# Kernel tuning notes

Measured on AMD Instinct MI355X. Metric: run time of the kernel, lower is better.

## Reference

```python
import jax, jax.numpy as jnp
import numpy as np

B, V, T = 256, 4, 512
N = 128          # num_notes_per_voice[0]
H = 256          # lstm_hidden_size
HL = 200         # hidden_size_linear
L = 2            # num_layers


def _scalar_lstm_last(x, Wih, Whh, b):
    """Stacked LSTM(input=1, hidden=1, layers=L) over x:(M,T) -> last output (M,).
    Wih, Whh, b: (L, 4) scalar weights per gate (i,f,g,o order, PyTorch biases summed)."""
    M = x.shape[0]
    h0 = jnp.zeros((L, M), x.dtype)
    c0 = jnp.zeros((L, M), x.dtype)

    def step(carry, xt):
        h, c = carry
        inp = xt
        hs, cs = [], []
        for l in range(L):
            g = Wih[l][:, None] * inp[None, :] + Whh[l][:, None] * h[l][None, :] + b[l][:, None]  # (4, M)
            i, f, gg, o = jax.nn.sigmoid(g[0]), jax.nn.sigmoid(g[1]), jnp.tanh(g[2]), jax.nn.sigmoid(g[3])
            cn = f * c[l] + i * gg
            hn = o * jnp.tanh(cn)
            hs.append(hn); cs.append(cn)
            inp = hn
        return (jnp.stack(hs), jnp.stack(cs)), None

    (h, _), _ = jax.lax.scan(step, (h0, c0), x.T)  # scan over time
    return h[-1]  # top layer final hidden, (M,)


def _lstm2_last(x, Wih0, Whh0, b0, Wih1, Whh1, b1):
    """2-layer LSTM(input=1, hidden=H) over x:(B,S,1) -> last top-layer hidden (B,H)."""
    Bs = x.shape[0]
    Hd = Whh0.shape[1]

    def cell(pre, c):
        i, f, g, o = jnp.split(pre, 4, axis=-1)
        cn = jax.nn.sigmoid(f) * c + jax.nn.sigmoid(i) * jnp.tanh(g)
        return jax.nn.sigmoid(o) * jnp.tanh(cn), cn

    z = jnp.zeros((Bs, Hd), x.dtype)

    def step(carry, xt):
        h0, c0, h1, c1 = carry
        h0n, c0n = cell(xt @ Wih0.T + h0 @ Whh0.T + b0, c0)
        h1n, c1n = cell(h0n @ Wih1.T + h1 @ Whh1.T + b1, c1)
        return (h0n, c0n, h1n, c1n), None

    (_, _, h1, _), _ = jax.lax.scan(step, (z, z, z, z), x.transpose(1, 0, 2))
    return h1


def _branch(tokens, tW, tU, tb, Wih0, Whh0, b0, Wih1, Whh1, b1):
    """Fused version of the per-class Python loop: one-hot each of N classes over
    time (voice 0 only, as in the source), run scalar LSTM per (batch, class),
    then 2-layer LSTM over the class axis. tokens: (B, T) int."""
    Bs, Ts = tokens.shape
    onehot = (tokens[:, :, None] == jnp.arange(N)[None, None, :]).astype(jnp.float32)  # (B,T,N)
    x = onehot.transpose(0, 2, 1).reshape(Bs * N, Ts)           # (B*N, T): one series per class
    states = _scalar_lstm_last(x, tW, tU, tb).reshape(Bs, N, 1)  # States_ln / States_rn
    return _lstm2_last(states, Wih0, Whh0, b0, Wih1, Whh1, b1)   # (B, H)


def setup_inputs() -> dict:
    key = jax.random.key(0)
    ks = iter(jax.random.split(key, 32))
    def rn_(shape, s=0.1):
        return jax.random.normal(next(ks), shape, dtype=jnp.float32) * s
    inp = {
        "ln": jax.random.randint(next(ks), (B, V, T), 0, N),
        "cn": jax.random.randint(next(ks), (B, V - 1), 0, N),
        "rn": jax.random.randint(next(ks), (B, V, T), 0, N),
        "metas": jax.random.randint(next(ks), (B, 3, T), 0, 16),
        # time_lstm_left/right: LSTM(1->1), L layers; biases summed into one
        "tl_Wih": rn_((L, 4), 0.5), "tl_Whh": rn_((L, 4), 0.5), "tl_b": rn_((L, 4), 0.5),
        "tr_Wih": rn_((L, 4), 0.5), "tr_Whh": rn_((L, 4), 0.5), "tr_b": rn_((L, 4), 0.5),
        # notes_lstm_left/right: 2-layer LSTM(1->H)
        "nl_Wih0": rn_((4 * H, 1)), "nl_Whh0": rn_((4 * H, H)), "nl_b0": rn_((4 * H,)),
        "nl_Wih1": rn_((4 * H, H)), "nl_Whh1": rn_((4 * H, H)), "nl_b1": rn_((4 * H,)),
        "nr_Wih0": rn_((4 * H, 1)), "nr_Whh0": rn_((4 * H, H)), "nr_b0": rn_((4 * H,)),
        "nr_Wih1": rn_((4 * H, H)), "nr_Whh1": rn_((4 * H, H)), "nr_b1": rn_((4 * H,)),
        # mlp_predictions: Linear(2H -> HL) -> ReLU -> Linear(HL -> N)
        "mW1": rn_((HL, 2 * H)), "mb1": rn_((HL,)),
        "mW2": rn_((N, HL)), "mb2": rn_((N,)),
    }
    return inp


def reference(ln, cn, rn, metas,
              tl_Wih, tl_Whh, tl_b, tr_Wih, tr_Whh, tr_b,
              nl_Wih0, nl_Whh0, nl_b0, nl_Wih1, nl_Whh1, nl_b1,
              nr_Wih0, nr_Whh0, nr_b0, nr_Wih1, nr_Whh1, nr_b1,
              mW1, mb1, mW2, mb2):
    # cn and metas are unpacked but unused in the original forward()
    note_pred_ln = _branch(ln[:, 0, :], tl_Wih, tl_Whh, tl_b,
                           nl_Wih0, nl_Whh0, nl_b0, nl_Wih1, nl_Whh1, nl_b1)
    note_pred_rn = _branch(rn[:, 0, :], tr_Wih, tr_Whh, tr_b,
                           nr_Wih0, nr_Whh0, nr_b0, nr_Wih1, nr_Whh1, nr_b1)
    h = jnp.concatenate([note_pred_ln, note_pred_rn], axis=1)   # (B, 2H)
    return jax.nn.relu(h @ mW1.T + mb1) @ mW2.T + mb2           # (B, N)
```

## Files before the change

### kernel.cpp

```cpp
#include <hip/hip_runtime.h>


typedef _Float16 f16;
typedef __attribute__((ext_vector_type(4))) _Float16 f16x4;
typedef __attribute__((ext_vector_type(8))) _Float16 f16x8;
typedef __attribute__((ext_vector_type(4))) float f32x4;
typedef unsigned long long u64;

#define NBATCH 256
#define NTIME  512
#define NCLS   128
#define NHID   256

__device__ __forceinline__ float sigf(float x) {
    return __builtin_amdgcn_rcpf(1.0f + __expf(-x));
}
__device__ __forceinline__ float tanh_f(float x) {
    return fmaf(2.0f, __builtin_amdgcn_rcpf(1.0f + __expf(-2.0f * x)), -1.0f);
}
__device__ __forceinline__ f16x4 LO(f16x8 v) { f16x4 r; r[0]=v[0]; r[1]=v[1]; r[2]=v[2]; r[3]=v[3]; return r; }
__device__ __forceinline__ f16x4 HI(f16x8 v) { f16x4 r; r[0]=v[4]; r[1]=v[5]; r[2]=v[6]; r[3]=v[7]; return r; }

__device__ __forceinline__ u64 ld_llc(const u64* p) {
    return __hip_atomic_load(p, __ATOMIC_RELAXED, __HIP_MEMORY_SCOPE_AGENT);
}
__device__ __forceinline__ void st_llc(u64* p, u64 v) {
    __hip_atomic_store(p, v, __ATOMIC_RELAXED, __HIP_MEMORY_SCOPE_AGENT);
}
__device__ __forceinline__ int ld_flag(const int* p) {
    return __hip_atomic_load(p, __ATOMIC_RELAXED, __HIP_MEMORY_SCOPE_AGENT);
}
__device__ __forceinline__ void st_flag(int* p, int v) {
    __hip_atomic_store(p, v, __ATOMIC_RELAXED, __HIP_MEMORY_SCOPE_AGENT);
}

struct P6 {
    const float* s0; const float* s1; const float* s2;
    const float* s3; const float* s4; const float* s5;
};

__global__ __launch_bounds__(256) void k_pre(
    const int* __restrict__ ln, const int* __restrict__ rn,
    const float* __restrict__ tlW, const float* __restrict__ tlU, const float* __restrict__ tlb,
    const float* __restrict__ trW, const float* __restrict__ trU, const float* __restrict__ trb,
    float* __restrict__ states,
    P6 p, f16* __restrict__ wdst,
    int* __restrict__ flags)
{
    const int bid = blockIdx.x;
    const int tid = threadIdx.x;
    if (bid >= 768) {
        int* f = flags + (bid - 768) * 16384;
        for (int i = tid; i < 16384; i += 256) f[i] = 0;
        return;
    }
    if (bid >= 256) {
        const int base = (bid - 256) * 3072;
#pragma unroll
        for (int k = 0; k < 12; ++k) {
            const int i = base + k * 256 + tid;
            const int seg = i >> 18, d = i & 262143;
            const float* s = seg == 0 ? p.s0 : seg == 1 ? p.s1 : seg == 2 ? p.s2
                           : seg == 3 ? p.s3 : seg == 4 ? p.s4 : p.s5;
            const int e  = d & 7;
            const int fr = (d >> 3) & 15;
            const int fq = (d >> 7) & 3;
            const int ktp = (d >> 9) & 7;
            const int fi = (d >> 12) & 15;
            const int g  = (d >> 16) & 3;
            const int row = g * 256 + fi * 16 + fr;
            const int col = ktp * 32 + (e >> 2) * 16 + fq * 4 + (e & 3);
            wdst[i] = (f16)s[row * 256 + col];
        }
        return;
    }
    __shared__ int tok[2][NTIME];
    const int half = tid >> 7, n = tid & 127;
    const int pair = bid * 2 + half;
    const int branch = pair >> 8;
    const int b = pair & 255;
    const int* tp = (branch ? rn : ln) + (size_t)b * (4 * NTIME);
    for (int i = n; i < NTIME; i += 128) tok[half][i] = tp[i];
    __syncthreads();
    const float* W  = branch ? trW : tlW;
    const float* U  = branch ? trU : tlU;
    const float* Bb = branch ? trb : tlb;
    const float u00 = U[0], u01 = U[1], u02 = U[2], u03 = U[3];
    const float f00 = Bb[0], f01 = Bb[1], f02 = Bb[2], f03 = Bb[3];
    const float o00 = f00 + W[0], o01 = f01 + W[1], o02 = f02 + W[2], o03 = f03 + W[3];
    const float w10 = W[4], w11 = W[5], w12 = W[6], w13 = W[7];
    const float u10 = U[4], u11 = U[5], u12 = U[6], u13 = U[7];
    const float b10 = Bb[4], b11 = Bb[5], b12 = Bb[6], b13 = Bb[7];
    float h0 = 0.f, c0 = 0.f, h1 = 0.f, c1 = 0.f;
    {
        const bool x = (tok[half][0] == n);
        float pi = fmaf(u00, h0, x ? o00 : f00);
        float pf = fmaf(u01, h0, x ? o01 : f01);
        float pg = fmaf(u02, h0, x ? o02 : f02);
        float po = fmaf(u03, h0, x ? o03 : f03);
        const float ig = sigf(pi), fg = sigf(pf), gg = tanh_f(pg), og = sigf(po);
        c0 = fmaf(fg, c0, ig * gg);
        h0 = og * tanh_f(c0);
    }
    for (int t = 1; t < NTIME; ++t) {
        const bool x = (tok[half][t] == n);
        float api = fmaf(u00, h0, x ? o00 : f00);
        float apf = fmaf(u01, h0, x ? o01 : f01);
        float apg = fmaf(u02, h0, x ? o02 : f02);
        float apo = fmaf(u03, h0, x ? o03 : f03);
        float bpi = fmaf(w10, h0, fmaf(u10, h1, b10));
        float bpf = fmaf(w11, h0, fmaf(u11, h1, b11));
        float bpg = fmaf(w12, h0, fmaf(u12, h1, b12));
        float bpo = fmaf(w13, h0, fmaf(u13, h1, b13));
        const float aig = sigf(api), afg = sigf(apf), agg = tanh_f(apg), aog = sigf(apo);
        const float big = sigf(bpi), bfg = sigf(bpf), bgg = tanh_f(bpg), bog = sigf(bpo);
        c0 = fmaf(afg, c0, aig * agg);
        c1 = fmaf(bfg, c1, big * bgg);
        h0 = aog * tanh_f(c0);
        h1 = bog * tanh_f(c1);
    }
    {
        float pi = fmaf(w10, h0, fmaf(u10, h1, b10));
        float pf = fmaf(w11, h0, fmaf(u11, h1, b11));
        float pg = fmaf(w12, h0, fmaf(u12, h1, b12));
        float po = fmaf(w13, h0, fmaf(u13, h1, b13));
        const float ig = sigf(pi), fg = sigf(pf), gg = tanh_f(pg), og = sigf(po);
        c1 = fmaf(fg, c1, ig * gg);
        h1 = og * tanh_f(c1);
    }
    states[((size_t)(branch * NBATCH + b)) * NCLS + n] = h1;
}

__global__ __launch_bounds__(256, 2) void k_rec(
    const float* __restrict__ states,
    const f16* __restrict__ whh0, const f16* __restrict__ whh1,
    const f16* __restrict__ wih1,
    const float* __restrict__ wih0L, const float* __restrict__ wih0R,
    const float* __restrict__ b0L, const float* __restrict__ b0R,
    const float* __restrict__ b1L, const float* __restrict__ b1R,
    f16* __restrict__ h0img,
    f16* __restrict__ ring,
    int* __restrict__ flags0,
    int* __restrict__ flags1,
    float* __restrict__ h1out)
{
    extern __shared__ char smem[];
    f16*   wlds = (f16*)smem;
    f16*   img  = (f16*)(smem + 65536);
    float* cmb  = (float*)(smem + 73728);

    const int bid = blockIdx.x;
    const bool isL1 = bid >= 256;
    const int sub = isL1 ? (bid - 256) : bid;
    const int qm = sub >> 5, g = sub & 31;
    const int branch = g >> 4, tb = g & 15;
    const int tid = threadIdx.x;
    const int w = tid >> 6, l = tid & 63, fr = l & 15, fq = l >> 4;

    {
        const f16* base = (isL1 ? whh1 : whh0) + ((size_t)branch << 18);
        for (int c = tid; c < 4096; c += 256) {
            const int rl = c >> 6, coli = c & 63;
            const int gg = rl >> 4, ff = (rl >> 3) & 1, ktp = rl & 7;
            *(uint4*)(wlds + rl * 512 + coli * 8) =
                *(const uint4*)(base + ((size_t)((gg * 16 + qm * 2 + ff) * 8 + ktp) << 9) + coli * 8);
        }
    }
    ((uint4*)img)[tid] = (uint4){0u, 0u, 0u, 0u};
    ((uint4*)img)[tid + 256] = (uint4){0u, 0u, 0u, 0u};

    if (!isL1) {
        const float* bias = branch ? b0R : b0L;
        const float* w0p  = branch ? wih0R : wih0L;
        const int fi_f = qm * 2 + (w < 2 ? w : 0);
        float bv[4], w0v[4];
#pragma unroll
        for (int g4 = 0; g4 < 4; ++g4) {
            bv[g4]  = bias[g4 * 256 + fi_f * 16 + fr];
            w0v[g4] = w0p[g4 * 256 + fi_f * 16 + fr];
        }
        float cst[4] = {0.f, 0.f, 0.f, 0.f};
        f16* gimg = h0img + (size_t)g * (NCLS * 4096);
        int* f0 = flags0 + g * 512;
        __syncthreads();

        for (int s = 0; s < NCLS; ++s) {
            float st[4];
            if (w < 2) {
#pragma unroll
                for (int r = 0; r < 4; ++r)
                    st[r] = states[((size_t)(branch * NBATCH + tb * 16 + fq * 4 + r)) * NCLS + s];
            }
            f16x4 af[16];
#pragma unroll
            for (int kt = 0; kt < 16; ++kt)
                af[kt] = *(const f16x4*)(img + kt * 256 + l * 4);
            f32x4 acc[2];
#pragma unroll
            for (int f = 0; f < 2; ++f) {
                f32x4 a0 = {0.f,0.f,0.f,0.f}, a1 = {0.f,0.f,0.f,0.f};
#pragma unroll
                for (int ktp = 0; ktp < 8; ++ktp) {
                    const f16x8 v = *(const f16x8*)(wlds + (((w * 2 + f) * 8 + ktp) << 9) + l * 8);
                    a0 = __builtin_amdgcn_mfma_f32_16x16x16f16(af[2 * ktp],     LO(v), a0, 0, 0, 0);
                    a1 = __builtin_amdgcn_mfma_f32_16x16x16f16(af[2 * ktp + 1], HI(v), a1, 0, 0, 0);
                }
                acc[f] = a0 + a1;
            }
            if (w == 0) {
#pragma unroll
                for (int r = 0; r < 4; ++r) cmb[(0 * 4 + r) * 64 + l] = acc[1][r];
            } else if (w == 1) {
#pragma unroll
                for (int r = 0; r < 4; ++r) cmb[(1 * 4 + r) * 64 + l] = acc[0][r];
            } else if (w == 2) {
#pragma unroll
                for (int r = 0; r < 4; ++r) {
                    cmb[(2 * 4 + r) * 64 + l] = acc[0][r];
                    cmb[(3 * 4 + r) * 64 + l] = acc[1][r];
                }
            } else {
#pragma unroll
                for (int r = 0; r < 4; ++r) {
                    cmb[(4 * 4 + r) * 64 + l] = acc[0][r];
                    cmb[(5 * 4 + r) * 64 + l] = acc[1][r];
                }
            }
            __syncthreads();
            if (w < 2) {
#pragma unroll
                for (int r = 0; r < 4; ++r) {
                    const float g0 = (w == 0) ? acc[0][r] : cmb[(0 * 4 + r) * 64 + l];
                    const float g1 = (w == 0) ? cmb[(1 * 4 + r) * 64 + l] : acc[1][r];
                    const float g2 = (w == 0) ? cmb[(2 * 4 + r) * 64 + l] : cmb[(3 * 4 + r) * 64 + l];
                    const float g3 = (w == 0) ? cmb[(4 * 4 + r) * 64 + l] : cmb[(5 * 4 + r) * 64 + l];
                    const float pi = fmaf(st[r], w0v[0], g0 + bv[0]);
                    const float pf = fmaf(st[r], w0v[1], g1 + bv[1]);
                    const float pg = fmaf(st[r], w0v[2], g2 + bv[2]);
                    const float po = fmaf(st[r], w0v[3], g3 + bv[3]);
                    const float ig = sigf(pi), fg = sigf(pf), gg = tanh_f(pg), og = sigf(po);
                    cst[r] = fmaf(fg, cst[r], ig * gg);
                    const float hn = og * tanh_f(cst[r]);
                    img[fi_f * 256 + (fq * 4 + r + 16 * (fr >> 2)) * 4 + (fr & 3)] = (f16)hn;
                }
            }
            __syncthreads();
            if (w == 0) {
                u64* gd = (u64*)(gimg + (size_t)s * 4096);
                st_llc(gd + qm * 128 + l,      ((const u64*)img)[qm * 128 + l]);
                st_llc(gd + qm * 128 + 64 + l, ((const u64*)img)[qm * 128 + 64 + l]);
                asm volatile("s_waitcnt vmcnt(0)" ::: "memory");
                if (l == 0) st_flag(f0 + qm * 64, s + 1);
                if (s < NCLS - 1 && l < 7) {
                    const int p = l + (l >= qm);
                    while (ld_flag(f0 + p * 64) <= s) __builtin_amdgcn_s_sleep(1);
                }
            }
            if (s == NCLS - 1) break;
            __syncthreads();
            if (tid < 128) {
                const u64* gs = (const u64*)(gimg + (size_t)s * 4096);
                u64 tmp[7];
#pragma unroll
                for (int j = 0; j < 7; ++j) {
                    const int p = j + (j >= qm);
                    tmp[j] = ld_llc(gs + p * 128 + tid);
                }
#pragma unroll
                for (int j = 0; j < 7; ++j) {
                    const int p = j + (j >= qm);
                    ((u64*)img)[p * 128 + tid] = tmp[j];
                }
            }
            __syncthreads();
        }
    } else {
        const float* bias = branch ? b1R : b1L;
        float bv[2][4];
#pragma unroll
        for (int f = 0; f < 2; ++f)
#pragma unroll
            for (int g4 = 0; g4 < 4; ++g4)
                bv[f][g4] = bias[g4 * 256 + (qm * 2 + f) * 16 + fr];
        float cst[2][4] = {{0.f,0.f,0.f,0.f},{0.f,0.f,0.f,0.f}};
        const f16* wstream = wih1 + ((size_t)branch << 18) + l * 8;
        const f16* gimg = h0img + (size_t)g * (NCLS * 4096);
        f16* gring = ring + (size_t)g * (4 * 4096);
        int* f0 = flags0 + g * 512;
        int* f1 = flags1 + g * 512;
        __syncthreads();
        if (w == 1 && l < 8) {
            while (ld_flag(f0 + l * 64) < 1) __builtin_amdgcn_s_sleep(2);
        }
        __syncthreads();
        f16x4 af0[16];
        {
            const u64* s2 = (const u64*)gimg + l;
#pragma unroll
            for (int kt = 0; kt < 16; ++kt)
                af0[kt] = __builtin_bit_cast(f16x4, ld_llc(s2 + kt * 64));
        }

        for (int t = 0; t < NCLS; ++t) {
            f16x8 wv[2][8];
#pragma unroll
            for (int f = 0; f < 2; ++f)
#pragma unroll
                for (int ktp = 0; ktp < 8; ++ktp)
                    wv[f][ktp] = *(const f16x8*)(wstream
                        + ((size_t)((w * 16 + qm * 2 + f) * 8 + ktp) << 9));
            f16x4 af1[16];
#pragma unroll
            for (int kt = 0; kt < 16; ++kt)
                af1[kt] = *(const f16x4*)(img + kt * 256 + l * 4);
            f32x4 acc[2];
#pragma unroll
            for (int f = 0; f < 2; ++f) {
                f32x4 a0 = {0.f,0.f,0.f,0.f}, a1 = {0.f,0.f,0.f,0.f};
#pragma unroll
                for (int ktp = 0; ktp < 8; ++ktp) {
                    const f16x8 v = *(const f16x8*)(wlds + (((w * 2 + f) * 8 + ktp) << 9) + l * 8);
                    a0 = __builtin_amdgcn_mfma_f32_16x16x16f16(af1[2 * ktp],     LO(v), a0, 0, 0, 0);
                    a1 = __builtin_amdgcn_mfma_f32_16x16x16f16(af1[2 * ktp + 1], HI(v), a1, 0, 0, 0);
                }
#pragma unroll
                for (int ktp = 0; ktp < 8; ++ktp) {
                    a0 = __builtin_amdgcn_mfma_f32_16x16x16f16(af0[2 * ktp],     LO(wv[f][ktp]), a0, 0, 0, 0);
                    a1 = __builtin_amdgcn_mfma_f32_16x16x16f16(af0[2 * ktp + 1], HI(wv[f][ktp]), a1, 0, 0, 0);
                }
                acc[f] = a0 + a1;
            }
            if (w > 0) {
#pragma unroll
                for (int f = 0; f < 2; ++f)
#pragma unroll
                    for (int r = 0; r < 4; ++r)
                        cmb[(((w - 1) * 2 + f) * 4 + r) * 64 + l] = acc[f][r];
            }
            __syncthreads();
            if (w == 0) {
#pragma unroll
                for (int f = 0; f < 2; ++f) {
#pragma unroll
                    for (int r = 0; r < 4; ++r) {
                        const float g0 = acc[f][r];
                        const float g1 = cmb[((0 * 2 + f) * 4 + r) * 64 + l];
                        const float g2 = cmb[((1 * 2 + f) * 4 + r) * 64 + l];
                        const float g3 = cmb[((2 * 2 + f) * 4 + r) * 64 + l];
                        const float pi = g0 + bv[f][0];
                        const float pf = g1 + bv[f][1];
                        const float pg = g2 + bv[f][2];
                        const float po = g3 + bv[f][3];
                        const float ig = sigf(pi), fg = sigf(pf), gg = tanh_f(pg), og = sigf(po);
                        cst[f][r] = fmaf(fg, cst[f][r], ig * gg);
                        const float hn = og * tanh_f(cst[f][r]);
                        if (t == NCLS - 1)
                            h1out[((size_t)(branch * NBATCH + tb * 16 + fq * 4 + r)) * NHID
                                  + (qm * 2 + f) * 16 + fr] = hn;
                        else
                            img[(qm * 2 + f) * 256 + (fq * 4 + r + 16 * (fr >> 2)) * 4 + (fr & 3)] = (f16)hn;
                    }
                }
            }
            if (t == NCLS - 1) break;
            f16* slot = gring + (size_t)(t & 3) * 4096;
            if (w == 0) {
                asm volatile("s_waitcnt lgkmcnt(0)" ::: "memory");
                u64* gd = (u64*)slot;
                st_llc(gd + qm * 128 + l,      ((const u64*)img)[qm * 128 + l]);
                st_llc(gd + qm * 128 + 64 + l, ((const u64*)img)[qm * 128 + 64 + l]);
                asm volatile("s_waitcnt vmcnt(0)" ::: "memory");
                if (l == 0) st_flag(f1 + qm * 64, t + 1);
                if (l < 7) {
                    const int p = l + (l >= qm);
                    while (ld_flag(f1 + p * 64) <= t) __builtin_amdgcn_s_sleep(1);
                }
            }
            if (w == 1 && l < 8) {
                while (ld_flag(f0 + l * 64) < t + 2) __builtin_amdgcn_s_sleep(1);
            }
            __syncthreads();
            {
                const u64* s2 = (const u64*)(gimg + (size_t)(t + 1) * 4096) + l;
#pragma unroll
                for (int kt = 0; kt < 16; ++kt)
                    af0[kt] = __builtin_bit_cast(f16x4, ld_llc(s2 + kt * 64));
            }
            if (tid < 128) {
                const u64* gs = (const u64*)slot;
                u64 tmp[7];
#pragma unroll
                for (int j = 0; j < 7; ++j) {
                    const int p = j + (j >= qm);
                    tmp[j] = ld_llc(gs + p * 128 + tid);
                }
#pragma unroll
                for (int j = 0; j < 7; ++j) {
                    const int p = j + (j >= qm);
                    ((u64*)img)[p * 128 + tid] = tmp[j];
                }
            }
            __syncthreads();
        }
    }
}

__global__ __launch_bounds__(256) void k_mlp(
    const float* __restrict__ h1all,
    const float* __restrict__ W1, const float* __restrict__ b1,
    const float* __restrict__ W2, const float* __restrict__ b2,
    float* __restrict__ out)
{
    __shared__ float hrow[512];
    __shared__ float hid[200];
    const int b = blockIdx.x, tid = threadIdx.x;
    hrow[tid]       = h1all[(size_t)b * NHID + tid];
    hrow[256 + tid] = h1all[(size_t)(NBATCH + b) * NHID + tid];
    __syncthreads();
    if (tid < 200) {
        float a = b1[tid];
        const float* wr = W1 + (size_t)tid * 512;
        for (int k = 0; k < 512; ++k) a = fmaf(wr[k], hrow[k], a);
        hid[tid] = fmaxf(a, 0.f);
    }
    __syncthreads();
    if (tid < 128) {
        float a = b2[tid];
        const float* wr = W2 + (size_t)tid * 200;
        for (int j = 0; j < 200; ++j) a = fmaf(wr[j], hid[j], a);
        out[(size_t)b * 128 + tid] = a;
    }
}

extern "C" void kernel_launch(void* const* d_in, const int* in_sizes, int n_in,
                              void* d_out, int out_size, void* d_ws, size_t ws_size,
                              hipStream_t stream)
{
    (void)in_sizes; (void)n_in; (void)out_size; (void)ws_size;
    const int*   ln    = (const int*)d_in[0];
    const int*   rn    = (const int*)d_in[2];
    const float* tlW   = (const float*)d_in[4];
    const float* tlU   = (const float*)d_in[5];
    const float* tlb   = (const float*)d_in[6];
    const float* trW   = (const float*)d_in[7];
    const float* trU   = (const float*)d_in[8];
    const float* trb   = (const float*)d_in[9];
    const float* wih0L = (const float*)d_in[10];
    const float* b0L   = (const float*)d_in[12];
    const float* b1L   = (const float*)d_in[15];
    const float* wih0R = (const float*)d_in[16];
    const float* b0R   = (const float*)d_in[18];
    const float* b1R   = (const float*)d_in[21];
    const float* mW1   = (const float*)d_in[22];
    const float* mb1   = (const float*)d_in[23];
    const float* mW2   = (const float*)d_in[24];
    const float* mb2   = (const float*)d_in[25];

    char* ws = (char*)d_ws;
    f16*   w16    = (f16*)ws;
    float* states = (float*)(ws + 3145728);
    float* h1out  = (float*)(ws + 3407872);
    int*   flags  = (int*)(ws + 3932160);
    f16*   ring   = (f16*)(ws + 4063232);
    f16*   h0img  = (f16*)(ws + 5111808);

    f16* whh0 = w16;
    f16* whh1 = w16 + 2 * 262144;
    f16* wih1 = w16 + 4 * 262144;
    int* flags0 = flags;
    int* flags1 = flags + 16384;

    (void)hipFuncSetAttribute(reinterpret_cast<const void*>(k_rec),
                              hipFuncAttributeMaxDynamicSharedMemorySize, 79872);

    P6 p { (const float*)d_in[11], (const float*)d_in[17],
           (const float*)d_in[14], (const float*)d_in[20],
           (const float*)d_in[13], (const float*)d_in[19] };
    k_pre<<<770, 256, 0, stream>>>(ln, rn, tlW, tlU, tlb, trW, trU, trb,
                                   states, p, w16, flags);
    k_rec<<<512, 256, 79872, stream>>>(states, whh0, whh1, wih1, wih0L, wih0R,
                                       b0L, b0R, b1L, b1R, h0img, ring,
                                       flags0, flags1, h1out);
    k_mlp<<<256, 256, 0, stream>>>(h1out, mW1, mb1, mW2, mb2, (float*)d_out);
}
```

Measured before the change: 640.1 us.

## Split layer-1 gate nonlinearity across two waves and move flag polling off the publisher

In the layer-1 LSTM loop, waves 0 and 1 now each compute the cell update for one of the two feature tiles, where wave 0 previously did both. The gate partial sums are exchanged through a rearranged shared-memory layout to support this. Flag polling for peer blocks moves from wave 0 to waves 2 and 3, so the publishing wave no longer also spins, and the layer-0 loop gets the same polling move. This shortens the serial per-step critical path at the cost of an extra __syncthreads per step.

```diff
diff --git a/kernel.cpp b/kernel.cpp
--- a/kernel.cpp
+++ b/kernel.cpp
@@ -251,10 +251,9 @@
                 st_llc(gd + qm * 128 + 64 + l, ((const u64*)img)[qm * 128 + 64 + l]);
                 asm volatile("s_waitcnt vmcnt(0)" ::: "memory");
                 if (l == 0) st_flag(f0 + qm * 64, s + 1);
-                if (s < NCLS - 1 && l < 7) {
-                    const int p = l + (l >= qm);
-                    while (ld_flag(f0 + p * 64) <= s) __builtin_amdgcn_s_sleep(1);
-                }
+            } else if (w == 2 && s < NCLS - 1 && l < 7) {
+                const int p = l + (l >= qm);
+                while (ld_flag(f0 + p * 64) <= s) __builtin_amdgcn_s_sleep(1);
             }
             if (s == NCLS - 1) break;
             __syncthreads();
@@ -276,20 +275,18 @@
         }
     } else {
         const float* bias = branch ? b1R : b1L;
-        float bv[2][4];
-#pragma unroll
-        for (int f = 0; f < 2; ++f)
-#pragma unroll
-            for (int g4 = 0; g4 < 4; ++g4)
-                bv[f][g4] = bias[g4 * 256 + (qm * 2 + f) * 16 + fr];
-        float cst[2][4] = {{0.f,0.f,0.f,0.f},{0.f,0.f,0.f,0.f}};
+        const int fi_f = qm * 2 + (w < 2 ? w : 0);
+        float bv[4];
+#pragma unroll
+        for (int g4 = 0; g4 < 4; ++g4) bv[g4] = bias[g4 * 256 + fi_f * 16 + fr];
+        float cst[4] = {0.f, 0.f, 0.f, 0.f};
         const f16* wstream = wih1 + ((size_t)branch << 18) + l * 8;
         const f16* gimg = h0img + (size_t)g * (NCLS * 4096);
         f16* gring = ring + (size_t)g * (4 * 4096);
         int* f0 = flags0 + g * 512;
         int* f1 = flags1 + g * 512;
         __syncthreads();
-        if (w == 1 && l < 8) {
+        if (w == 3 && l < 8) {
             while (ld_flag(f0 + l * 64) < 1) __builtin_amdgcn_s_sleep(2);
         }
         __syncthreads();
@@ -330,53 +327,60 @@
                 }
                 acc[f] = a0 + a1;
             }
-            if (w > 0) {
-#pragma unroll
-                for (int f = 0; f < 2; ++f)
-#pragma unroll
-                    for (int r = 0; r < 4; ++r)
-                        cmb[(((w - 1) * 2 + f) * 4 + r) * 64 + l] = acc[f][r];
-            }
-            __syncthreads();
             if (w == 0) {
 #pragma unroll
-                for (int f = 0; f < 2; ++f) {
-#pragma unroll
-                    for (int r = 0; r < 4; ++r) {
-                        const float g0 = acc[f][r];
-                        const float g1 = cmb[((0 * 2 + f) * 4 + r) * 64 + l];
-                        const float g2 = cmb[((1 * 2 + f) * 4 + r) * 64 + l];
-                        const float g3 = cmb[((2 * 2 + f) * 4 + r) * 64 + l];
-                        const float pi = g0 + bv[f][0];
-                        const float pf = g1 + bv[f][1];
-                        const float pg = g2 + bv[f][2];
-                        const float po = g3 + bv[f][3];
-                        const float ig = sigf(pi), fg = sigf(pf), gg = tanh_f(pg), og = sigf(po);
-                        cst[f][r] = fmaf(fg, cst[f][r], ig * gg);
-                        const float hn = og * tanh_f(cst[f][r]);
-                        if (t == NCLS - 1)
-                            h1out[((size_t)(branch * NBATCH + tb * 16 + fq * 4 + r)) * NHID
-                                  + (qm * 2 + f) * 16 + fr] = hn;
-                        else
-                            img[(qm * 2 + f) * 256 + (fq * 4 + r + 16 * (fr >> 2)) * 4 + (fr & 3)] = (f16)hn;
-                    }
+                for (int r = 0; r < 4; ++r) cmb[(3 * 4 + r) * 64 + l] = acc[1][r];
+            } else if (w == 1) {
+#pragma unroll
+                for (int r = 0; r < 4; ++r) cmb[(0 * 4 + r) * 64 + l] = acc[0][r];
+            } else if (w == 2) {
+#pragma unroll
+                for (int r = 0; r < 4; ++r) {
+                    cmb[(1 * 4 + r) * 64 + l] = acc[0][r];
+                    cmb[(4 * 4 + r) * 64 + l] = acc[1][r];
+                }
+            } else {
+#pragma unroll
+                for (int r = 0; r < 4; ++r) {
+                    cmb[(2 * 4 + r) * 64 + l] = acc[0][r];
+                    cmb[(5 * 4 + r) * 64 + l] = acc[1][r];
+                }
+            }
+            __syncthreads();
+            if (w < 2) {
+#pragma unroll
+                for (int r = 0; r < 4; ++r) {
+                    const float g0 = (w == 0) ? acc[0][r] : cmb[(3 * 4 + r) * 64 + l];
+                    const float g1 = (w == 0) ? cmb[(0 * 4 + r) * 64 + l] : acc[1][r];
+                    const float g2 = (w == 0) ? cmb[(1 * 4 + r) * 64 + l] : cmb[(4 * 4 + r) * 64 + l];
+                    const float g3 = (w == 0) ? cmb[(2 * 4 + r) * 64 + l] : cmb[(5 * 4 + r) * 64 + l];
+                    const float pi = g0 + bv[0];
+                    const float pf = g1 + bv[1];
+                    const float pg = g2 + bv[2];
+                    const float po = g3 + bv[3];
+                    const float ig = sigf(pi), fg = sigf(pf), gg = tanh_f(pg), og = sigf(po);
+                    cst[r] = fmaf(fg, cst[r], ig * gg);
+                    const float hn = og * tanh_f(cst[r]);
+                    if (t == NCLS - 1)
+                        h1out[((size_t)(branch * NBATCH + tb * 16 + fq * 4 + r)) * NHID
+                              + fi_f * 16 + fr] = hn;
+                    else
+                        img[fi_f * 256 + (fq * 4 + r + 16 * (fr >> 2)) * 4 + (fr & 3)] = (f16)hn;
                 }
             }
             if (t == NCLS - 1) break;
+            __syncthreads();
             f16* slot = gring + (size_t)(t & 3) * 4096;
             if (w == 0) {
-                asm volatile("s_waitcnt lgkmcnt(0)" ::: "memory");
                 u64* gd = (u64*)slot;
                 st_llc(gd + qm * 128 + l,      ((const u64*)img)[qm * 128 + l]);
                 st_llc(gd + qm * 128 + 64 + l, ((const u64*)img)[qm * 128 + 64 + l]);
                 asm volatile("s_waitcnt vmcnt(0)" ::: "memory");
                 if (l == 0) st_flag(f1 + qm * 64, t + 1);
-                if (l < 7) {
-                    const int p = l + (l >= qm);
-                    while (ld_flag(f1 + p * 64) <= t) __builtin_amdgcn_s_sleep(1);
-                }
-            }
-            if (w == 1 && l < 8) {
+            } else if (w == 2 && l < 7) {
+                const int p = l + (l >= qm);
+                while (ld_flag(f1 + p * 64) <= t) __builtin_amdgcn_s_sleep(1);
+            } else if (w == 3 && l < 8) {
                 while (ld_flag(f0 + l * 64) < t + 2) __builtin_amdgcn_s_sleep(1);
             }
             __syncthreads();
```

Result: faster. 602.0 us (-6.0%).
